# Optimization experiments

Measured on AMD Instinct MI355X. Metric: run time of the kernel, lower is better.

## Reference

```python
import jax, jax.numpy as jnp
import numpy as np

WS, SS, P, H = 7, 3, 14, 12  # window, shift, patch grid, heads
NW = (P // WS) ** 2          # windows per image = 4
N_WIN = WS * WS              # tokens per window = 49

def _rel_pos_index():
    coords = np.stack(np.meshgrid(np.arange(WS), np.arange(WS), indexing='ij')).reshape(2, -1)
    rel = (coords[:, :, None] - coords[:, None, :]).transpose(1, 2, 0).astype(np.int64)
    rel[..., 0] += WS - 1
    rel[..., 1] += WS - 1
    rel[..., 0] *= 2 * WS - 1
    return rel.sum(-1)  # [49,49]

def _shift_mask():
    img = np.zeros((P, P))
    sl = (slice(0, -WS), slice(-WS, -SS), slice(-SS, None))
    cnt = 0
    for h in sl:
        for w in sl:
            img[h, w] = cnt
            cnt += 1
    mw = img.reshape(P // WS, WS, P // WS, WS).transpose(0, 2, 1, 3).reshape(-1, N_WIN)
    am = mw[:, None, :] - mw[:, :, None]
    return np.where(am != 0, -100.0, 0.0).astype(np.float32)  # [nW,49,49]

RPI = jnp.asarray(_rel_pos_index())
MASK = jnp.asarray(_shift_mask())

def _hswish(x):
    return x * jnp.clip(x + 3.0, 0.0, 6.0) / 6.0

def _hsig(x):
    return jnp.clip(x + 3.0, 0.0, 6.0) / 6.0

def _bn(x, g, b, eps=1e-5):
    # training-mode batchnorm over (B,H,W) per channel, biased variance
    m = x.mean((0, 2, 3), keepdims=True)
    v = ((x - m) ** 2).mean((0, 2, 3), keepdims=True)
    return (x - m) / jnp.sqrt(v + eps) * g[None, :, None, None] + b[None, :, None, None]

def setup_inputs() -> dict:
    key = jax.random.key(0)
    ks = jax.random.split(key, 20)
    C, HID = 768, 3072
    return {
        'x': jax.random.normal(ks[0], (32, 197, C), jnp.float32),
        'w_qkv': jax.random.normal(ks[1], (3 * C, C), jnp.float32) * 0.02,
        'w_proj': jax.random.normal(ks[2], (C, C), jnp.float32) * 0.02,
        'b_proj': jax.random.normal(ks[3], (C,), jnp.float32) * 0.02,
        'rpb_table': jax.random.normal(ks[4], ((2 * WS - 1) ** 2, H), jnp.float32) * 0.02,
        'pw1_w': jax.random.normal(ks[5], (HID, C), jnp.float32) * 0.02,
        'bn1_g': 1.0 + jax.random.normal(ks[6], (HID,), jnp.float32) * 0.02,
        'bn1_b': jax.random.normal(ks[7], (HID,), jnp.float32) * 0.02,
        'dw_w': jax.random.normal(ks[8], (HID, 3, 3), jnp.float32) * 0.1,
        'bn2_g': 1.0 + jax.random.normal(ks[9], (HID,), jnp.float32) * 0.02,
        'bn2_b': jax.random.normal(ks[10], (HID,), jnp.float32) * 0.02,
        'se_w1': jax.random.normal(ks[11], (HID // 4, HID), jnp.float32) * 0.02,
        'se_b1': jax.random.normal(ks[12], (HID // 4,), jnp.float32) * 0.02,
        'se_w2': jax.random.normal(ks[13], (HID, HID // 4), jnp.float32) * 0.02,
        'se_b2': jax.random.normal(ks[14], (HID,), jnp.float32) * 0.02,
        'pw2_w': jax.random.normal(ks[15], (C, HID), jnp.float32) * 0.02,
        'bn3_g': 1.0 + jax.random.normal(ks[16], (C,), jnp.float32) * 0.02,
        'bn3_b': jax.random.normal(ks[17], (C,), jnp.float32) * 0.02,
    }

def reference(x, w_qkv, w_proj, b_proj, rpb_table, pw1_w, bn1_g, bn1_b, dw_w,
              bn2_g, bn2_b, se_w1, se_b1, se_w2, se_b2, pw2_w, bn3_g, bn3_b):
    B, N, C = x.shape
    hd = C // H
    scale = hd ** -0.5
    nw = P // WS

    cls_tok = x[:, :1]
    xs = x[:, 1:].reshape(B, P, P, C)
    xs = jnp.roll(xs, (-SS, -SS), axis=(1, 2))  # cyclic shift
    # window partition -> [B*nW, 49, C]
    win = xs.reshape(B, nw, WS, nw, WS, C).transpose(0, 1, 3, 2, 4, 5).reshape(B * NW, N_WIN, C)

    qkv = (win @ w_qkv.T).reshape(B * NW, N_WIN, 3, H, hd).transpose(2, 0, 3, 1, 4)
    q, k, v = qkv[0], qkv[1], qkv[2]  # [B*nW, H, 49, hd]
    attn = jnp.einsum('bhqd,bhkd->bhqk', q, k) * scale
    # relative position bias gather: [H,49,49]
    bias = rpb_table[RPI.reshape(-1)].reshape(N_WIN, N_WIN, H).transpose(2, 0, 1)
    attn = attn + bias[None]
    # shifted-window mask add
    attn = (attn.reshape(B, NW, H, N_WIN, N_WIN) + MASK[None, :, None]).reshape(B * NW, H, N_WIN, N_WIN)
    attn = jax.nn.softmax(attn, axis=-1)
    out = jnp.einsum('bhqk,bhkd->bhqd', attn, v).transpose(0, 2, 1, 3).reshape(B * NW, N_WIN, C)
    out = out @ w_proj.T + b_proj

    # window reverse + reverse shift
    xs = out.reshape(B, nw, nw, WS, WS, C).transpose(0, 1, 3, 2, 4, 5).reshape(B, P, P, C)
    xs = jnp.roll(xs, (SS, SS), axis=(1, 2))
    x = jnp.concatenate([cls_tok, xs.reshape(B, P * P, C)], axis=1)

    # LocalityFeedForward (inverted residual conv MLP with SE)
    cls_tok, xt = x[:, :1], x[:, 1:]
    f = xt.transpose(0, 2, 1).reshape(B, C, P, P)
    h = _hswish(_bn(jnp.einsum('bchw,oc->bohw', f, pw1_w), bn1_g, bn1_b))
    h = _hswish(_bn(jax.lax.conv_general_dilated(
        h, dw_w[:, None], (1, 1), 'SAME',
        feature_group_count=h.shape[1],
        dimension_numbers=('NCHW', 'OIHW', 'NCHW')), bn2_g, bn2_b))
    s = h.mean((2, 3))  # global avg pool [B, hid]
    s = _hsig(jax.nn.relu(s @ se_w1.T + se_b1) @ se_w2.T + se_b2)
    h = h * s[:, :, None, None]
    h = _bn(jnp.einsum('bchw,oc->bohw', h, pw2_w), bn3_g, bn3_b)
    f = f + h
    x = jnp.concatenate([cls_tok, f.reshape(B, C, P * P).transpose(0, 2, 1)], axis=1)
    return x
```

## Files before the change

### kernel.cpp

```cpp
#include <hip/hip_runtime.h>
#include <hip/hip_bf16.h>

typedef unsigned short ushort_t;
typedef unsigned int uint_t;
typedef short short8 __attribute__((ext_vector_type(8)));
typedef float floatx4 __attribute__((ext_vector_type(4)));

__device__ inline float b2f(ushort_t u){
    uint_t v = ((uint_t)u) << 16;
    return __uint_as_float(v);
}
__device__ inline ushort_t f2b(float f){
    uint_t v = __float_as_uint(f);
    uint_t r = (v + 0x7FFFu + ((v >> 16) & 1u)) >> 16;
    return (ushort_t)r;
}
__device__ inline void unpack8(uint4 u, float* f){
    uint_t w[4] = {u.x, u.y, u.z, u.w};
    #pragma unroll
    for (int i = 0; i < 4; ++i){
        f[2*i]   = __uint_as_float(w[i] << 16);
        f[2*i+1] = __uint_as_float(w[i] & 0xFFFF0000u);
    }
}
__device__ inline uint4 pack8(const float* f){
    uint4 o;
    uint_t w[4];
    #pragma unroll
    for (int i = 0; i < 4; ++i)
        w[i] = (uint_t)f2b(f[2*i]) | ((uint_t)f2b(f[2*i+1]) << 16);
    o.x = w[0]; o.y = w[1]; o.z = w[2]; o.w = w[3];
    return o;
}
__device__ inline ushort4 cvt4(float4 v){
    ushort4 o;
    o.x = f2b(v.x); o.y = f2b(v.y); o.z = f2b(v.z); o.w = f2b(v.w);
    return o;
}
__device__ inline float hswish(float y){
    return y * fminf(fmaxf(y + 3.f, 0.f), 6.f) * (1.f/6.f);
}

#define MROWS 6272
#define CDIM  768
#define HID   3072
#define QKV3  2304

__device__ inline int scatter_row(int ri){
    int w  = ri / 49, t = ri % 49;
    int b  = w >> 2,  wi = w & 3;
    int wy = wi >> 1, wx = wi & 1;
    int ty = t / 7,   tx = t % 7;
    int yd = (wy*7 + ty + 3) % 14;
    int xd = (wx*7 + tx + 3) % 14;
    return b*196 + yd*14 + xd;
}

__device__ inline void bn_coef(const float* __restrict__ sums, int Cch,
                               const float* __restrict__ g, const float* __restrict__ b,
                               int c, float& sc, float& sh){
    float mean = sums[c] * (1.f/6272.f);
    float var  = sums[Cch + c] * (1.f/6272.f) - mean*mean;
    float s = g[c] * rsqrtf(var + 1e-5f);
    sc = s;
    sh = b[c] - mean*s;
}

__global__ __launch_bounds__(256) void prep_k(const float4* __restrict__ x,
                                              const float4* __restrict__ w_qkv,
                                              const float4* __restrict__ w_proj,
                                              const float4* __restrict__ pw1_w,
                                              const float4* __restrict__ pw2_w,
                                              const float* __restrict__ dw_w,
                                              const float* __restrict__ rpb,
                                              float* __restrict__ sums1,
                                              float* __restrict__ sums23,
                                              float* __restrict__ dwwT,
                                              ushort4* __restrict__ wqkvb,
                                              ushort4* __restrict__ wprojb,
                                              ushort4* __restrict__ pw1b,
                                              ushort4* __restrict__ pw2b,
                                              ushort4* __restrict__ win,
                                              float* __restrict__ bm){
    int bid = blockIdx.x;
    const int t = threadIdx.x;
    if (bid < 24){ int i = bid*256 + t; if (i < 2*HID) sums1[i] = 0.f; return; }
    bid -= 24;
    if (bid < 30){ int i = bid*256 + t; if (i < 2*HID + 2*CDIM) sums23[i] = 0.f; return; }
    bid -= 30;
    if (bid < 108){
        int i = bid*256 + t;
        if (i < HID*9){ int c = i/9, k = i%9; dwwT[k*HID + c] = dw_w[i]; }
        return;
    }
    bid -= 108;
    if (bid < 1728){ int i = bid*256 + t; wqkvb[i] = cvt4(w_qkv[i]); return; }
    bid -= 1728;
    if (bid < 576){ int i = bid*256 + t; wprojb[i] = cvt4(w_proj[i]); return; }
    bid -= 576;
    if (bid < 2304){ int i = bid*256 + t; pw1b[i] = cvt4(pw1_w[i]); return; }
    bid -= 2304;
    if (bid < 2304){ int i = bid*256 + t; pw2b[i] = cvt4(pw2_w[i]); return; }
    bid -= 2304;
    if (bid < 4704){
        int idx = bid*256 + t;
        int r  = idx / 192, c4 = idx % 192;
        int w  = r / 49,  tt = r % 49;
        int b  = w >> 2,  wi = w & 3;
        int wy = wi >> 1, wx = wi & 1;
        int ty = tt / 7,  tx = tt % 7;
        int ys = (wy*7 + ty + 3) % 14;
        int xs = (wx*7 + tx + 3) % 14;
        win[idx] = cvt4(x[(size_t)b*197*192 + (size_t)(1 + ys*14 + xs)*192 + c4]);
        return;
    }
    bid -= 4704;
    {
        int idx = bid*256 + t;
        int ki = idx & 63, qi = (idx >> 6) & 63, wi = (idx >> 12) & 3, h = idx >> 14;
        float v = -1e30f;
        if (qi < 49 && ki < 49){
            int qy = qi/7, qx = qi%7, ky = ki/7, kx = ki%7;
            int ridx = (qy - ky + 6)*13 + (qx - kx + 6);
            v = rpb[ridx*12 + h];
            int wy = wi >> 1, wx = wi & 1;
            int gqy = wy*7 + qy, gqx = wx*7 + qx, gky = wy*7 + ky, gkx = wx*7 + kx;
            int cq = ((gqy < 7) ? 0 : (gqy < 11 ? 1 : 2))*3 + ((gqx < 7) ? 0 : (gqx < 11 ? 1 : 2));
            int ck = ((gky < 7) ? 0 : (gky < 11 ? 1 : 2))*3 + ((gkx < 7) ? 0 : (gkx < 11 ? 1 : 2));
            if (cq != ck) v -= 100.f;
        }
        bm[idx] = v;
    }
}

__global__ __launch_bounds__(256) void gemm_bt(const ushort_t* __restrict__ A,
                                               const ushort_t* __restrict__ B,
                                               ushort_t* __restrict__ Cb,
                                               float* __restrict__ Cf,
                                               int M, int N, int K,
                                               const float* __restrict__ bias,
                                               float* __restrict__ stats,
                                               int scat){
    const int nx   = gridDim.x;
    int flat = blockIdx.y * nx + blockIdx.x;
    int xcd  = flat & 7;
    int k    = flat >> 3;
    int by   = xcd + 8 * (k / nx);
    int bx   = k % nx;
    if (by * 128 >= M) return;

    __shared__ __align__(16) ushort_t As[2][128*32];
    __shared__ __align__(16) ushort_t Bs[2][128*32];
    const int tid  = threadIdx.x;
    const int lane = tid & 63;
    const int wid  = tid >> 6;
    const int m0 = by * 128;
    const int n0 = bx * 128;
    const int wm = (wid >> 1) * 64;
    const int wn = (wid & 1) * 64;

    const int srow = (lane >> 2);
    const int scol = (((lane & 3) ^ ((lane >> 3) & 3)) * 8);

    floatx4 acc[4][4] = {};

    auto stage = [&](int buf, int k0){
        #pragma unroll
        for (int j = 0; j < 2; ++j){
            int ch  = wid*2 + j;
            const ushort_t* gA = A + (size_t)(m0 + ch*16 + srow)*K + k0 + scol;
            const ushort_t* gB = B + (size_t)(n0 + ch*16 + srow)*K + k0 + scol;
            __builtin_amdgcn_global_load_lds(
                (const __attribute__((address_space(1))) void*)gA,
                (__attribute__((address_space(3))) void*)(&As[buf][ch*512 + lane*8]), 16, 0, 0);
            __builtin_amdgcn_global_load_lds(
                (const __attribute__((address_space(1))) void*)gB,
                (__attribute__((address_space(3))) void*)(&Bs[buf][ch*512 + lane*8]), 16, 0, 0);
        }
    };

    const int NK = K >> 5;
    stage(0, 0);

    const int fr   = lane & 15;
    const int quad = lane >> 4;
    const int cosw = (quad ^ ((fr >> 1) & 3)) * 8;
    int cur = 0;
    for (int it = 0; it < NK; ++it){
        __builtin_amdgcn_sched_barrier(0);
        __builtin_amdgcn_s_barrier();
        if (it + 1 < NK){
            stage(cur ^ 1, (it + 1) << 5);
            asm volatile("s_waitcnt vmcnt(4)" ::: "memory");
        } else {
            asm volatile("s_waitcnt vmcnt(0)" ::: "memory");
        }
        __builtin_amdgcn_s_barrier();
        __builtin_amdgcn_sched_barrier(0);

        short8 af[4], bfr[4];
        #pragma unroll
        for (int i = 0; i < 4; ++i){
            af[i]  = *(const short8*)(&As[cur][(wm + i*16 + fr)*32 + cosw]);
            bfr[i] = *(const short8*)(&Bs[cur][(wn + i*16 + fr)*32 + cosw]);
        }
        #pragma unroll
        for (int i = 0; i < 4; ++i)
            #pragma unroll
            for (int j = 0; j < 4; ++j)
                acc[i][j] = __builtin_amdgcn_mfma_f32_16x16x32_bf16(af[i], bfr[j], acc[i][j], 0, 0, 0);
        cur ^= 1;
    }

    if (!scat && Cb){
        __syncthreads();
        ushort_t* Cspace = (wid < 2) ? &As[0][0] : &Bs[0][0];
        #pragma unroll
        for (int i = 0; i < 4; ++i){
            #pragma unroll
            for (int j = 0; j < 4; ++j){
                int col = wn + j*16 + fr;
                float bv = bias ? bias[n0 + col] : 0.f;
                #pragma unroll
                for (int r = 0; r < 4; ++r)
                    Cspace[(i*16 + quad*4 + r)*128 + (col ^ (quad << 4))] =
                        f2b(acc[i][j][r] + bv);
            }
        }
        __syncthreads();
        #pragma unroll
        for (int q = 0; q < 8; ++q){
            int fl  = q*256 + tid;
            int row = fl >> 4, u4c = fl & 15;
            const ushort_t* srcRow = (row < 64) ? (&As[0][0] + row*128)
                                                : (&Bs[0][0] + (row - 64)*128);
            int g = (row >> 2) & 3;
            *(uint4*)(Cb + (size_t)(m0 + row)*N + n0 + u4c*8) =
                *(const uint4*)(srcRow + ((u4c*8) ^ (g << 4)));
        }
    } else {
        #pragma unroll
        for (int i = 0; i < 4; ++i){
            int grow = m0 + wm + i*16 + quad*4;
            #pragma unroll
            for (int j = 0; j < 4; ++j){
                int gcol = n0 + wn + j*16 + fr;
                float bv = bias ? bias[gcol] : 0.f;
                if (scat){
                    #pragma unroll
                    for (int r = 0; r < 4; ++r){
                        float v = acc[i][j][r] + bv;
                        size_t off = (size_t)scatter_row(grow + r)*N + gcol;
                        if (Cf) Cf[off] = v;
                        Cb[off] = f2b(v);
                    }
                } else {
                    #pragma unroll
                    for (int r = 0; r < 4; ++r)
                        Cf[(size_t)(grow + r)*N + gcol] = acc[i][j][r] + bv;
                }
            }
        }
    }

    if (stats){
        #pragma unroll
        for (int j = 0; j < 4; ++j){
            int gcol = n0 + wn + j*16 + fr;
            float bv = bias ? bias[gcol] : 0.f;
            float sv = 0.f, sq = 0.f;
            #pragma unroll
            for (int i = 0; i < 4; ++i)
                #pragma unroll
                for (int r = 0; r < 4; ++r){
                    float v = acc[i][j][r] + bv;
                    sv += v; sq += v*v;
                }
            sv += __shfl_xor(sv, 16, 64);  sq += __shfl_xor(sq, 16, 64);
            sv += __shfl_xor(sv, 32, 64);  sq += __shfl_xor(sq, 32, 64);
            if (lane < 16){
                atomicAdd(&stats[gcol], sv);
                atomicAdd(&stats[N + gcol], sq);
            }
        }
    }
}

__global__ __launch_bounds__(256) void gemm_bt64(const ushort_t* __restrict__ A,
                                                 const ushort_t* __restrict__ B,
                                                 ushort_t* __restrict__ Cb,
                                                 float* __restrict__ Cf,
                                                 int M, int N, int K,
                                                 const float* __restrict__ bias,
                                                 float* __restrict__ stats,
                                                 int scat){
    const int nx   = gridDim.x;
    int flat = blockIdx.y * nx + blockIdx.x;
    int xcd  = flat & 7;
    int k    = flat >> 3;
    int by   = xcd + 8 * (k / nx);
    int bx   = k % nx;
    if (by * 128 >= M) return;

    __shared__ __align__(16) ushort_t As[2][128*32];
    __shared__ __align__(16) ushort_t Bs[2][64*32];
    const int tid  = threadIdx.x;
    const int lane = tid & 63;
    const int wid  = tid >> 6;
    const int m0 = by * 128;
    const int n0 = bx * 64;
    const int wm = (wid >> 1) * 64;
    const int wn = (wid & 1) * 32;

    const int srow = (lane >> 2);
    const int scol = (((lane & 3) ^ ((lane >> 3) & 3)) * 8);

    floatx4 acc[4][2] = {};

    auto stage = [&](int buf, int k0){
        #pragma unroll
        for (int j = 0; j < 2; ++j){
            int ch = wid*2 + j;
            const ushort_t* gA = A + (size_t)(m0 + ch*16 + srow)*K + k0 + scol;
            __builtin_amdgcn_global_load_lds(
                (const __attribute__((address_space(1))) void*)gA,
                (__attribute__((address_space(3))) void*)(&As[buf][ch*512 + lane*8]), 16, 0, 0);
        }
        const ushort_t* gB = B + (size_t)(n0 + wid*16 + srow)*K + k0 + scol;
        __builtin_amdgcn_global_load_lds(
            (const __attribute__((address_space(1))) void*)gB,
            (__attribute__((address_space(3))) void*)(&Bs[buf][wid*512 + lane*8]), 16, 0, 0);
    };

    const int NK = K >> 5;
    stage(0, 0);

    const int fr   = lane & 15;
    const int quad = lane >> 4;
    const int cosw = (quad ^ ((fr >> 1) & 3)) * 8;
    int cur = 0;
    for (int it = 0; it < NK; ++it){
        __builtin_amdgcn_sched_barrier(0);
        __builtin_amdgcn_s_barrier();
        if (it + 1 < NK){
            stage(cur ^ 1, (it + 1) << 5);
            asm volatile("s_waitcnt vmcnt(3)" ::: "memory");
        } else {
            asm volatile("s_waitcnt vmcnt(0)" ::: "memory");
        }
        __builtin_amdgcn_s_barrier();
        __builtin_amdgcn_sched_barrier(0);

        short8 af[4], bfr[2];
        #pragma unroll
        for (int i = 0; i < 4; ++i)
            af[i]  = *(const short8*)(&As[cur][(wm + i*16 + fr)*32 + cosw]);
        #pragma unroll
        for (int j = 0; j < 2; ++j)
            bfr[j] = *(const short8*)(&Bs[cur][(wn + j*16 + fr)*32 + cosw]);
        #pragma unroll
        for (int i = 0; i < 4; ++i)
            #pragma unroll
            for (int j = 0; j < 2; ++j)
                acc[i][j] = __builtin_amdgcn_mfma_f32_16x16x32_bf16(af[i], bfr[j], acc[i][j], 0, 0, 0);
        cur ^= 1;
    }

    if (Cb){
        __syncthreads();
        ushort_t* Cst = &As[0][0];
        #pragma unroll
        for (int i = 0; i < 4; ++i){
            #pragma unroll
            for (int j = 0; j < 2; ++j){
                int col = wn + j*16 + fr;
                float bv = bias ? bias[n0 + col] : 0.f;
                #pragma unroll
                for (int r = 0; r < 4; ++r)
                    Cst[(wm + i*16 + quad*4 + r)*64 + (col ^ (quad << 4))] =
                        f2b(acc[i][j][r] + bv);
            }
        }
        __syncthreads();
        #pragma unroll
        for (int q = 0; q < 4; ++q){
            int fl  = q*256 + tid;
            int row = fl >> 3, u4c = fl & 7;
            int g = (row >> 2) & 3;
            int orow = scat ? scatter_row(m0 + row) : (m0 + row);
            *(uint4*)(Cb + (size_t)orow*N + n0 + u4c*8) =
                *(const uint4*)(Cst + row*64 + ((u4c*8) ^ (g << 4)));
        }
    } else {
        #pragma unroll
        for (int i = 0; i < 4; ++i){
            int grow = m0 + wm + i*16 + quad*4;
            #pragma unroll
            for (int j = 0; j < 2; ++j){
                int gcol = n0 + wn + j*16 + fr;
                float bv = bias ? bias[gcol] : 0.f;
                #pragma unroll
                for (int r = 0; r < 4; ++r)
                    Cf[(size_t)(grow + r)*N + gcol] = acc[i][j][r] + bv;
            }
        }
    }

    if (stats){
        #pragma unroll
        for (int j = 0; j < 2; ++j){
            int gcol = n0 + wn + j*16 + fr;
            float bv = bias ? bias[gcol] : 0.f;
            float sv = 0.f, sq = 0.f;
            #pragma unroll
            for (int i = 0; i < 4; ++i)
                #pragma unroll
                for (int r = 0; r < 4; ++r){
                    float v = acc[i][j][r] + bv;
                    sv += v; sq += v*v;
                }
            sv += __shfl_xor(sv, 16, 64);  sq += __shfl_xor(sq, 16, 64);
            sv += __shfl_xor(sv, 32, 64);  sq += __shfl_xor(sq, 32, 64);
            if (lane < 16){
                atomicAdd(&stats[gcol], sv);
                atomicAdd(&stats[N + gcol], sq);
            }
        }
    }
}

__global__ __launch_bounds__(256) void attn_mfma(const ushort_t* __restrict__ qkv,
                                                 ushort_t* __restrict__ outp,
                                                 const float* __restrict__ bm){
    __shared__ __align__(16) ushort_t Ps[64*72];
    __shared__ __align__(16) ushort_t VT[64*72];
    const int tid = threadIdx.x, lane = tid & 63, wid = tid >> 6;
    const int h = blockIdx.x, w = blockIdx.y, wi = w & 3;
    const int fr = lane & 15, quad = lane >> 4, co = quad*8;

    for (int idx = tid; idx < 64*8; idx += 256){
        int k = idx >> 3, ng = idx & 7;
        uint4 u = {0u, 0u, 0u, 0u};
        if (k < 49) u = *(const uint4*)(qkv + (size_t)(w*49 + k)*QKV3 + 1536 + h*64 + ng*8);
        const ushort_t* vp = (const ushort_t*)&u;
        #pragma unroll
        for (int e = 0; e < 8; ++e) VT[(ng*8 + e)*72 + k] = vp[e];
    }
    __syncthreads();

    floatx4 accs[4] = {};
    const ushort_t* qbase = qkv + (size_t)(w*49 + wid*16 + fr)*QKV3 + h*64;
    #pragma unroll
    for (int k0 = 0; k0 < 64; k0 += 32){
        short8 af = *(const short8*)(qbase + k0 + co);
        #pragma unroll
        for (int j = 0; j < 4; ++j){
            const ushort_t* kbase = qkv + (size_t)(w*49 + j*16 + fr)*QKV3 + 768 + h*64;
            short8 bf = *(const short8*)(kbase + k0 + co);
            accs[j] = __builtin_amdgcn_mfma_f32_16x16x32_bf16(af, bf, accs[j], 0, 0, 0);
        }
    }

    const float* bmh = bm + (size_t)((h*4 + wi)*64 + wid*16)*64;
    #pragma unroll
    for (int r = 0; r < 4; ++r){
        int lrow = quad*4 + r;
        float m = -3e38f;
        #pragma unroll
        for (int j = 0; j < 4; ++j){
            float a = accs[j][r]*0.125f + bmh[lrow*64 + j*16 + fr];
            accs[j][r] = a;
            m = fmaxf(m, a);
        }
        #pragma unroll
        for (int off = 1; off < 16; off <<= 1) m = fmaxf(m, __shfl_xor(m, off, 64));
        float s = 0.f;
        #pragma unroll
        for (int j = 0; j < 4; ++j){
            float e = __expf(accs[j][r] - m);
            accs[j][r] = e; s += e;
        }
        #pragma unroll
        for (int off = 1; off < 16; off <<= 1) s += __shfl_xor(s, off, 64);
        float inv = 1.f / s;
        #pragma unroll
        for (int j = 0; j < 4; ++j)
            Ps[(wid*16 + lrow)*72 + j*16 + fr] = f2b(accs[j][r]*inv);
    }
    __syncthreads();

    floatx4 acco[4] = {};
    #pragma unroll
    for (int k0 = 0; k0 < 64; k0 += 32){
        short8 af = *(const short8*)(Ps + (wid*16 + fr)*72 + k0 + co);
        #pragma unroll
        for (int j = 0; j < 4; ++j){
            short8 bf = *(const short8*)(VT + (j*16 + fr)*72 + k0 + co);
            acco[j] = __builtin_amdgcn_mfma_f32_16x16x32_bf16(af, bf, acco[j], 0, 0, 0);
        }
    }
    __syncthreads();
    #pragma unroll
    for (int r = 0; r < 4; ++r){
        int orow = wid*16 + quad*4 + r;
        #pragma unroll
        for (int j = 0; j < 4; ++j)
            Ps[orow*72 + j*16 + fr] = f2b(acco[j][r]);
    }
    __syncthreads();
    for (int it = tid; it < 49*8; it += 256){
        int row = it >> 3, u4c = it & 7;
        *(uint4*)(outp + (size_t)(w*49 + row)*CDIM + h*64 + u4c*8) =
            *(const uint4*)(Ps + row*72 + u4c*8);
    }
}

__global__ __launch_bounds__(256) void dwconv_s(const ushort_t* __restrict__ in,
                                                const float* __restrict__ wT,
                                                const float* __restrict__ sums1,
                                                const float* __restrict__ g1,
                                                const float* __restrict__ b1,
                                                ushort_t* __restrict__ out,
                                                float* __restrict__ sums2){
    const int cgl = threadIdx.x & 31;
    const int rp  = threadIdx.x >> 5;
    const int cg  = blockIdx.x*32 + cgl;
    const int c   = cg*8;
    const int r0  = blockIdx.y*112;
    float sc[8], sh[8];
    #pragma unroll
    for (int e = 0; e < 8; ++e) bn_coef(sums1, HID, g1, b1, c+e, sc[e], sh[e]);
    float wv[9][8];
    #pragma unroll
    for (int kk = 0; kk < 9; ++kk){
        const float4* wp = (const float4*)(wT + kk*HID + c);
        float4 w0 = wp[0], w1 = wp[1];
        wv[kk][0]=w0.x; wv[kk][1]=w0.y; wv[kk][2]=w0.z; wv[kk][3]=w0.w;
        wv[kk][4]=w1.x; wv[kk][5]=w1.y; wv[kk][6]=w1.z; wv[kk][7]=w1.w;
    }
    float s[8] = {}, q[8] = {};
    for (int r = r0 + rp; r < r0 + 112; r += 8){
        int b = r / 196, p = r % 196;
        int y = p / 14,  x = p % 14;
        const uint4* inb = (const uint4*)(in + (size_t)b*196*HID);
        float acc[8] = {};
        #pragma unroll
        for (int ky = 0; ky < 3; ++ky){
            int yy = y + ky - 1;
            if ((unsigned)yy >= 14u) continue;
            #pragma unroll
            for (int kx = 0; kx < 3; ++kx){
                int xx = x + kx - 1;
                if ((unsigned)xx >= 14u) continue;
                uint4 u = inb[(yy*14 + xx)*384 + cg];
                float fin[8]; unpack8(u, fin);
                #pragma unroll
                for (int e = 0; e < 8; ++e)
                    acc[e] += hswish(fin[e]*sc[e] + sh[e]) * wv[ky*3 + kx][e];
            }
        }
        ((uint4*)out)[(size_t)r*384 + cg] = pack8(acc);
        #pragma unroll
        for (int e = 0; e < 8; ++e){ s[e] += acc[e]; q[e] += acc[e]*acc[e]; }
    }
    #pragma unroll
    for (int e = 0; e < 8; ++e){
        s[e] += __shfl_xor(s[e], 32, 64);
        q[e] += __shfl_xor(q[e], 32, 64);
    }
    __shared__ float red[4][32][17];
    const int wvv = threadIdx.x >> 6;
    if ((threadIdx.x & 32) == 0){
        #pragma unroll
        for (int e = 0; e < 8; ++e){
            red[wvv][cgl][e]   = s[e];
            red[wvv][cgl][8+e] = q[e];
        }
    }
    __syncthreads();
    #pragma unroll
    for (int k = 0; k < 2; ++k){
        int o = threadIdx.x*2 + k;
        int cgo = o >> 4, e = o & 15;
        float v = red[0][cgo][e] + red[1][cgo][e] + red[2][cgo][e] + red[3][cgo][e];
        int cc = blockIdx.x*256 + cgo*8 + (e & 7);
        atomicAdd(&sums2[(e < 8 ? 0 : HID) + cc], v);
    }
}

__global__ __launch_bounds__(256) void se_mean_v(const ushort_t* __restrict__ X,
                                                 const float* __restrict__ sums2,
                                                 const float* __restrict__ g2,
                                                 const float* __restrict__ b2,
                                                 float* __restrict__ s){
    const int b   = blockIdx.x;
    const int cgl = threadIdx.x & 31;
    const int rp  = threadIdx.x >> 5;
    const int cg  = blockIdx.y*32 + cgl;
    const int c   = cg*8;
    float sc[8], sh[8];
    #pragma unroll
    for (int e = 0; e < 8; ++e) bn_coef(sums2, HID, g2, b2, c+e, sc[e], sh[e]);
    const uint4* Xb = (const uint4*)(X + (size_t)b*196*HID);
    float a[8] = {};
    for (int p = rp; p < 196; p += 8){
        uint4 u = Xb[(size_t)p*384 + cg];
        float f[8]; unpack8(u, f);
        #pragma unroll
        for (int e = 0; e < 8; ++e) a[e] += hswish(f[e]*sc[e] + sh[e]);
    }
    #pragma unroll
    for (int e = 0; e < 8; ++e) a[e] += __shfl_xor(a[e], 32, 64);
    __shared__ float red[4][32][9];
    const int wv = threadIdx.x >> 6;
    if ((threadIdx.x & 32) == 0){
        #pragma unroll
        for (int e = 0; e < 8; ++e) red[wv][cgl][e] = a[e];
    }
    __syncthreads();
    {
        int o = threadIdx.x;
        int cgo = o >> 3, e = o & 7;
        float v = red[0][cgo][e] + red[1][cgo][e] + red[2][cgo][e] + red[3][cgo][e];
        s[(size_t)b*HID + blockIdx.y*256 + cgo*8 + e] = v * (1.f/196.f);
    }
}
__global__ __launch_bounds__(256) void se_fc(const float* __restrict__ in,
                                             const float* __restrict__ w,
                                             const float* __restrict__ bias,
                                             float* __restrict__ out,
                                             int IN, int OUT, int mode){
    int wv   = (blockIdx.x*256 + threadIdx.x) >> 6;
    int lane = threadIdx.x & 63;
    if (wv >= OUT) return;
    const float* wr = w + (size_t)wv * IN;
    float acc[32];
    #pragma unroll
    for (int b = 0; b < 32; ++b) acc[b] = 0.f;
    for (int k = lane; k < IN; k += 64){
        float wval = wr[k];
        #pragma unroll
        for (int b = 0; b < 32; ++b)
            acc[b] += in[b*IN + k] * wval;
    }
    #pragma unroll
    for (int b = 0; b < 32; ++b){
        float v = acc[b];
        #pragma unroll
        for (int off = 32; off; off >>= 1) v += __shfl_down(v, off, 64);
        if (lane == 0){
            float a = v + bias[wv];
            if (mode == 0) a = fmaxf(a, 0.f);
            else           a = fminf(fmaxf(a + 3.f, 0.f), 6.f) * (1.f/6.f);
            out[b*OUT + wv] = a;
        }
    }
}
__global__ __launch_bounds__(256) void se_scale(ushort_t* __restrict__ X,
                                                const float* __restrict__ sums2,
                                                const float* __restrict__ g2,
                                                const float* __restrict__ b2,
                                                const float* __restrict__ s2){
    int idx = blockIdx.x*256 + threadIdx.x;
    if (idx >= MROWS * (HID/8)) return;
    int r = idx / (HID/8), c8 = idx % (HID/8);
    int b = r / 196;
    int c = c8*8;
    uint4 u = ((uint4*)X)[idx];
    float f[8]; unpack8(u, f);
    const float* sp = s2 + b*HID + c;
    #pragma unroll
    for (int e = 0; e < 8; ++e){
        float sc, sh;
        bn_coef(sums2, HID, g2, b2, c+e, sc, sh);
        f[e] = hswish(f[e]*sc + sh) * sp[e];
    }
    ((uint4*)X)[idx] = pack8(f);
}

__global__ __launch_bounds__(256) void final_k(const float4* __restrict__ xin,
                                               const ushort_t* __restrict__ fb,
                                               const ushort_t* __restrict__ hb4,
                                               const float* __restrict__ sums3,
                                               const float* __restrict__ g3,
                                               const float* __restrict__ b3,
                                               float4* __restrict__ outp){
    int idx = blockIdx.x*256 + threadIdx.x;
    if (idx >= 32*197*96) return;
    int b = idx / (197*96);
    int rem = idx % (197*96);
    int n = rem / 96, c8 = rem % 96;
    size_t obase = ((size_t)b*197 + n)*192 + c8*2;
    if (n == 0){
        outp[obase]     = xin[obase];
        outp[obase + 1] = xin[obase + 1];
        return;
    }
    size_t off = ((size_t)b*196 + n - 1)*96 + c8;
    uint4 fu = ((const uint4*)fb)[off];
    uint4 hu = ((const uint4*)hb4)[off];
    float fv[8], hv[8];
    unpack8(fu, fv); unpack8(hu, hv);
    int c = c8*8;
    float o[8];
    #pragma unroll
    for (int e = 0; e < 8; ++e){
        float sc, sh;
        bn_coef(sums3, CDIM, g3, b3, c+e, sc, sh);
        o[e] = fv[e] + hv[e]*sc + sh;
    }
    float4 o0 = {o[0], o[1], o[2], o[3]};
    float4 o1 = {o[4], o[5], o[6], o[7]};
    outp[obase]     = o0;
    outp[obase + 1] = o1;
}

extern "C" void kernel_launch(void* const* d_in, const int* in_sizes, int n_in,
                              void* d_out, int out_size, void* d_ws, size_t ws_size,
                              hipStream_t stream){
    const float* x      = (const float*)d_in[0];
    const float* w_qkv  = (const float*)d_in[1];
    const float* w_proj = (const float*)d_in[2];
    const float* b_proj = (const float*)d_in[3];
    const float* rpb    = (const float*)d_in[4];
    const float* pw1_w  = (const float*)d_in[5];
    const float* bn1_g  = (const float*)d_in[6];
    const float* bn1_b  = (const float*)d_in[7];
    const float* dw_w   = (const float*)d_in[8];
    const float* bn2_g  = (const float*)d_in[9];
    const float* bn2_b  = (const float*)d_in[10];
    const float* se_w1  = (const float*)d_in[11];
    const float* se_b1  = (const float*)d_in[12];
    const float* se_w2  = (const float*)d_in[13];
    const float* se_b2  = (const float*)d_in[14];
    const float* pw2_w  = (const float*)d_in[15];
    const float* bn3_g  = (const float*)d_in[16];
    const float* bn3_b  = (const float*)d_in[17];

    char* ws = (char*)d_ws;
    ushort_t* win    = (ushort_t*)(ws + 0);
    ushort_t* hb     = (ushort_t*)(ws + 0);
    ushort_t* qkv    = (ushort_t*)(ws + 9633792);
    ushort_t* wqkvb  = (ushort_t*)(ws + 38535168);
    ushort_t* attnb  = (ushort_t*)(ws + 38535168);
    ushort_t* ha     = (ushort_t*)(ws + 38535168);
    ushort_t* hb4    = (ushort_t*)(ws + 38535168);
    ushort_t* wprojb = (ushort_t*)(ws + 48168960);
    float*    bm     = (float*)(ws + 49348608);
    ushort_t* fb2    = (ushort_t*)(ws + 77070336);
    float*    sums2  = (float*)(ws + 86704128);
    float*    sums3  = (float*)(ws + 86728704);
    ushort_t* pw1b   = (ushort_t*)(ws + 86734848);
    ushort_t* pw2b   = (ushort_t*)(ws + 91453440);
    float*    sums1  = (float*)(ws + 96337920);
    float*    s      = (float*)(ws + 96362496);
    float*    s1     = (float*)(ws + 96755712);
    float*    s2     = (float*)(ws + 96854016);
    float*    dwwT   = (float*)(ws + 96854016);

    const int vec_hid8 = (MROWS*(HID/8) + 255)/256;
    const int GY = 56;

    prep_k<<<12546, 256, 0, stream>>>((const float4*)x, (const float4*)w_qkv,
                                      (const float4*)w_proj, (const float4*)pw1_w,
                                      (const float4*)pw2_w, dw_w, rpb,
                                      sums1, sums2, dwwT,
                                      (ushort4*)wqkvb, (ushort4*)wprojb,
                                      (ushort4*)pw1b, (ushort4*)pw2b,
                                      (ushort4*)win, bm);

    gemm_bt<<<dim3(QKV3/128, GY), 256, 0, stream>>>(win, wqkvb, qkv, nullptr, MROWS, QKV3, CDIM, nullptr, nullptr, 0);
    attn_mfma<<<dim3(12, 128), 256, 0, stream>>>(qkv, attnb, bm);
    gemm_bt64<<<dim3(CDIM/64, GY), 256, 0, stream>>>(attnb, wprojb, fb2, nullptr, MROWS, CDIM, CDIM, b_proj, nullptr, 1);

    gemm_bt<<<dim3(HID/128, GY), 256, 0, stream>>>(fb2, pw1b, ha, nullptr, MROWS, HID, CDIM, nullptr, sums1, 0);
    dwconv_s<<<dim3(12, GY), 256, 0, stream>>>(ha, dwwT, sums1, bn1_g, bn1_b, hb, sums2);
    se_mean_v<<<dim3(32, 12), 256, 0, stream>>>(hb, sums2, bn2_g, bn2_b, s);
    se_fc<<<dim3((CDIM*64)/256), 256, 0, stream>>>(s, se_w1, se_b1, s1, HID, CDIM, 0);
    se_fc<<<dim3((HID*64)/256), 256, 0, stream>>>(s1, se_w2, se_b2, s2, CDIM, HID, 1);
    se_scale<<<vec_hid8, 256, 0, stream>>>(hb, sums2, bn2_g, bn2_b, s2);

    gemm_bt64<<<dim3(CDIM/64, GY), 256, 0, stream>>>(hb, pw2b, hb4, nullptr, MROWS, CDIM, HID, nullptr, sums3, 0);
    final_k<<<(32*197*96 + 255)/256, 256, 0, stream>>>((const float4*)x, fb2, hb4, sums3, bn3_g, bn3_b, (float4*)d_out);
}
```

Baseline: 496.7 us.

## Use 256x128 tiles with 512 threads for QKV and pw1 GEMMs

Replaces the 128x128-tile, 256-thread GEMM with a 256x128-tile, 512-thread variant used for the QKV projection and the first pointwise conv. Each block now stages twice as many A rows per B tile, which cuts B-tile reloads and the number of blocks. Rows past M are clamped on load and masked on store and in the stats. The epilogue writes through LDS in two halves, with the bias and scatter paths dropped. The larger tile leaves more out-of-range rows at the M edge and lowers the block count, which risks worse load balance across CUs.

```diff
diff --git a/kernel.cpp b/kernel.cpp
--- a/kernel.cpp
+++ b/kernel.cpp
@@ -133,28 +133,25 @@
     }
 }
 
-__global__ __launch_bounds__(256) void gemm_bt(const ushort_t* __restrict__ A,
-                                               const ushort_t* __restrict__ B,
-                                               ushort_t* __restrict__ Cb,
-                                               float* __restrict__ Cf,
-                                               int M, int N, int K,
-                                               const float* __restrict__ bias,
-                                               float* __restrict__ stats,
-                                               int scat){
+__global__ __launch_bounds__(512) void gemm256_32(const ushort_t* __restrict__ A,
+                                                  const ushort_t* __restrict__ B,
+                                                  ushort_t* __restrict__ Cb,
+                                                  int M, int N, int K,
+                                                  float* __restrict__ stats){
     const int nx   = gridDim.x;
     int flat = blockIdx.y * nx + blockIdx.x;
     int xcd  = flat & 7;
     int k    = flat >> 3;
     int by   = xcd + 8 * (k / nx);
     int bx   = k % nx;
-    if (by * 128 >= M) return;
-
-    __shared__ __align__(16) ushort_t As[2][128*32];
+    if (by * 256 >= M) return;
+
+    __shared__ __align__(16) ushort_t As[2][256*32];
     __shared__ __align__(16) ushort_t Bs[2][128*32];
     const int tid  = threadIdx.x;
     const int lane = tid & 63;
     const int wid  = tid >> 6;
-    const int m0 = by * 128;
+    const int m0 = by * 256;
     const int n0 = bx * 128;
     const int wm = (wid >> 1) * 64;
     const int wn = (wid & 1) * 64;
@@ -168,15 +165,17 @@
         #pragma unroll
         for (int j = 0; j < 2; ++j){
             int ch  = wid*2 + j;
-            const ushort_t* gA = A + (size_t)(m0 + ch*16 + srow)*K + k0 + scol;
-            const ushort_t* gB = B + (size_t)(n0 + ch*16 + srow)*K + k0 + scol;
+            int row = m0 + ch*16 + srow;
+            if (row > M-1) row = M-1;
+            const ushort_t* gA = A + (size_t)row*K + k0 + scol;
             __builtin_amdgcn_global_load_lds(
                 (const __attribute__((address_space(1))) void*)gA,
                 (__attribute__((address_space(3))) void*)(&As[buf][ch*512 + lane*8]), 16, 0, 0);
-            __builtin_amdgcn_global_load_lds(
-                (const __attribute__((address_space(1))) void*)gB,
-                (__attribute__((address_space(3))) void*)(&Bs[buf][ch*512 + lane*8]), 16, 0, 0);
-        }
+        }
+        const ushort_t* gB = B + (size_t)(n0 + wid*16 + srow)*K + k0 + scol;
+        __builtin_amdgcn_global_load_lds(
+            (const __attribute__((address_space(1))) void*)gB,
+            (__attribute__((address_space(3))) void*)(&Bs[buf][wid*512 + lane*8]), 16, 0, 0);
     };
 
     const int NK = K >> 5;
@@ -191,7 +190,7 @@
         __builtin_amdgcn_s_barrier();
         if (it + 1 < NK){
             stage(cur ^ 1, (it + 1) << 5);
-            asm volatile("s_waitcnt vmcnt(4)" ::: "memory");
+            asm volatile("s_waitcnt vmcnt(3)" ::: "memory");
         } else {
             asm volatile("s_waitcnt vmcnt(0)" ::: "memory");
         }
@@ -212,70 +211,55 @@
         cur ^= 1;
     }
 
-    if (!scat && Cb){
-        __syncthreads();
-        ushort_t* Cspace = (wid < 2) ? &As[0][0] : &Bs[0][0];
-        #pragma unroll
-        for (int i = 0; i < 4; ++i){
+    __syncthreads();
+    ushort_t* Cs = &As[0][0];
+    #pragma unroll
+    for (int p = 0; p < 2; ++p){
+        if ((wid >> 2) == p){
+            int lr0 = wm - p*128;
             #pragma unroll
-            for (int j = 0; j < 4; ++j){
-                int col = wn + j*16 + fr;
-                float bv = bias ? bias[n0 + col] : 0.f;
+            for (int i = 0; i < 4; ++i){
                 #pragma unroll
-                for (int r = 0; r < 4; ++r)
-                    Cspace[(i*16 + quad*4 + r)*128 + (col ^ (quad << 4))] =
-                        f2b(acc[i][j][r] + bv);
-            }
-        }
-        __syncthreads();
-        #pragma unroll
-        for (int q = 0; q < 8; ++q){
-            int fl  = q*256 + tid;
-            int row = fl >> 4, u4c = fl & 15;
-            const ushort_t* srcRow = (row < 64) ? (&As[0][0] + row*128)
-                                                : (&Bs[0][0] + (row - 64)*128);
-            int g = (row >> 2) & 3;
-            *(uint4*)(Cb + (size_t)(m0 + row)*N + n0 + u4c*8) =
-                *(const uint4*)(srcRow + ((u4c*8) ^ (g << 4)));
-        }
-    } else {
-        #pragma unroll
-        for (int i = 0; i < 4; ++i){
-            int grow = m0 + wm + i*16 + quad*4;
-            #pragma unroll
-            for (int j = 0; j < 4; ++j){
-                int gcol = n0 + wn + j*16 + fr;
-                float bv = bias ? bias[gcol] : 0.f;
-                if (scat){
-                    #pragma unroll
-                    for (int r = 0; r < 4; ++r){
-                        float v = acc[i][j][r] + bv;
-                        size_t off = (size_t)scatter_row(grow + r)*N + gcol;
-                        if (Cf) Cf[off] = v;
-                        Cb[off] = f2b(v);
-                    }
-                } else {
+                for (int j = 0; j < 4; ++j){
+                    int col = wn + j*16 + fr;
                     #pragma unroll
                     for (int r = 0; r < 4; ++r)
-                        Cf[(size_t)(grow + r)*N + gcol] = acc[i][j][r] + bv;
+                        Cs[(lr0 + i*16 + quad*4 + r)*128 + (col ^ (quad << 4))] =
+                            f2b(acc[i][j][r]);
                 }
             }
         }
+        __syncthreads();
+        #pragma unroll
+        for (int q = 0; q < 4; ++q){
+            int fl  = q*512 + tid;
+            int row = fl >> 4, u4c = fl & 15;
+            int grow = m0 + p*128 + row;
+            if (grow < M){
+                int g = (row >> 2) & 3;
+                *(uint4*)(Cb + (size_t)grow*N + n0 + u4c*8) =
+                    *(const uint4*)(Cs + row*128 + ((u4c*8) ^ (g << 4)));
+            }
+        }
+        __syncthreads();
     }
 
     if (stats){
         #pragma unroll
         for (int j = 0; j < 4; ++j){
             int gcol = n0 + wn + j*16 + fr;
-            float bv = bias ? bias[gcol] : 0.f;
             float sv = 0.f, sq = 0.f;
             #pragma unroll
-            for (int i = 0; i < 4; ++i)
+            for (int i = 0; i < 4; ++i){
+                int grow = m0 + wm + i*16 + quad*4;
                 #pragma unroll
                 for (int r = 0; r < 4; ++r){
-                    float v = acc[i][j][r] + bv;
-                    sv += v; sq += v*v;
+                    if (grow + r < M){
+                        float v = acc[i][j][r];
+                        sv += v; sq += v*v;
+                    }
                 }
+            }
             sv += __shfl_xor(sv, 16, 64);  sq += __shfl_xor(sq, 16, 64);
             sv += __shfl_xor(sv, 32, 64);  sq += __shfl_xor(sq, 32, 64);
             if (lane < 16){
@@ -760,6 +744,7 @@
 
     const int vec_hid8 = (MROWS*(HID/8) + 255)/256;
     const int GY = 56;
+    const int GY256 = 32;
 
     prep_k<<<12546, 256, 0, stream>>>((const float4*)x, (const float4*)w_qkv,
                                       (const float4*)w_proj, (const float4*)pw1_w,
@@ -769,11 +754,11 @@
                                       (ushort4*)pw1b, (ushort4*)pw2b,
                                       (ushort4*)win, bm);
 
-    gemm_bt<<<dim3(QKV3/128, GY), 256, 0, stream>>>(win, wqkvb, qkv, nullptr, MROWS, QKV3, CDIM, nullptr, nullptr, 0);
+    gemm256_32<<<dim3(QKV3/128, GY256), 512, 0, stream>>>(win, wqkvb, qkv, MROWS, QKV3, CDIM, nullptr);
     attn_mfma<<<dim3(12, 128), 256, 0, stream>>>(qkv, attnb, bm);
     gemm_bt64<<<dim3(CDIM/64, GY), 256, 0, stream>>>(attnb, wprojb, fb2, nullptr, MROWS, CDIM, CDIM, b_proj, nullptr, 1);
 
-    gemm_bt<<<dim3(HID/128, GY), 256, 0, stream>>>(fb2, pw1b, ha, nullptr, MROWS, HID, CDIM, nullptr, sums1, 0);
+    gemm256_32<<<dim3(HID/128, GY256), 512, 0, stream>>>(fb2, pw1b, ha, MROWS, HID, CDIM, sums1);
     dwconv_s<<<dim3(12, GY), 256, 0, stream>>>(ha, dwwT, sums1, bn1_g, bn1_b, hb, sums2);
     se_mean_v<<<dim3(32, 12), 256, 0, stream>>>(hb, sums2, bn2_g, bn2_b, s);
     se_fc<<<dim3((CDIM*64)/256), 256, 0, stream>>>(s, se_w1, se_b1, s1, HID, CDIM, 0);
```

After: 494.9 us. No clear change (-0.4%).
